# Kernel tuning notes

Measured on AMD Instinct MI355X. Metric: run time of the kernel, lower is better.

The kernel has to match this reference:

```python
import jax, jax.numpy as jnp
import numpy as np

H = 1024      # hidden_dim == memory_dim (required by seq-axis concat)
M = 1024      # memory_dim
FF = 4096     # ff_dim
WIN = 16      # window_size
SLOTS = 10    # persistent memory slots
B, S = 2, 4096
EPS_LN = 1e-5
EPS_NORM = 1e-12


def _layernorm(x, g, b):
    m = jnp.mean(x, axis=-1, keepdims=True)
    v = jnp.var(x, axis=-1, keepdims=True)
    return (x - m) / jnp.sqrt(v + EPS_LN) * g + b


def setup_inputs() -> dict:
    key = jax.random.key(0)
    ks = jax.random.split(key, 12)

    def lin_w(k, out_d, in_d):
        return jax.random.normal(k, (out_d, in_d), jnp.float32) / np.sqrt(in_d)

    return {
        "x": jax.random.normal(ks[0], (B, S, H), jnp.float32),
        "mem_W": lin_w(ks[1], M, M), "mem_b": jnp.zeros((M,), jnp.float32),
        "P": jax.random.normal(ks[2], (SLOTS, M), jnp.float32),
        "Wi": lin_w(ks[3], M, H), "bi": jnp.zeros((M,), jnp.float32),
        "Wl1": lin_w(ks[4], M, M), "bl1": jnp.zeros((M,), jnp.float32),
        "Wl2": lin_w(ks[5], M, M), "bl2": jnp.zeros((M,), jnp.float32),
        "Wo": lin_w(ks[6], H, M), "bo": jnp.zeros((H,), jnp.float32),
        "fgate": jnp.ones((1,), jnp.float32),
        "lrate": jnp.ones((1,), jnp.float32),
        "Wg": lin_w(ks[7], H, 2 * H), "bg": jnp.zeros((H,), jnp.float32),
        "W1": lin_w(ks[8], FF, H), "b1": jnp.zeros((FF,), jnp.float32),
        "W2": lin_w(ks[9], H, FF), "b2": jnp.zeros((H,), jnp.float32),
        "g1": jnp.ones((H,), jnp.float32), "be1": jnp.zeros((H,), jnp.float32),
        "g2": jnp.ones((H,), jnp.float32), "be2": jnp.zeros((H,), jnp.float32),
        "g3": jnp.ones((H,), jnp.float32), "be3": jnp.zeros((H,), jnp.float32),
    }


def reference(x, mem_W, mem_b, P, Wi, bi, Wl1, bl1, Wl2, bl2, Wo, bo,
              fgate, lrate, Wg, bg, W1, b1, W2, b2,
              g1, be1, g2, be2, g3, be3):
    b, s, h = x.shape
    # k = concat(x, persistent) along seq; v = k.clone()
    k_full = jnp.concatenate([x, jnp.broadcast_to(P, (b,) + P.shape)], axis=1)  # [B, S+SLOTS, H]

    # sit at positions >= S and are never inside the window, so only x is attended.
    idx = jnp.arange(s)[:, None] + jnp.arange(-WIN, 1)[None, :]
    valid = idx >= 0
    k_win = k_full[:, jnp.maximum(idx, 0)]
    scores = jnp.einsum('bsh,bswh->bsw', x, k_win) * (h ** -0.5)
    scores = jnp.where(valid[None], scores, -jnp.inf)
    attn_out = jnp.einsum('bsw,bswh->bsh', jax.nn.softmax(scores, axis=-1), k_win)
    x1 = _layernorm(x + attn_out, g1, be1)

    # --- neural long-term memory (key == value since v = k.clone())
    kv = k_full.reshape(-1, h)
    kn = kv / jnp.maximum(jnp.linalg.norm(kv, axis=-1, keepdims=True), EPS_NORM)
    kp = kn @ Wi.T + bi          # projected key; value_proj is identical
    vp = kp
    hdd = jax.nn.silu(kp @ Wl1.T + bl1)
    hdd = jax.nn.silu(hdd @ Wl2.T + bl2)
    pred = hdd @ mem_W.T + mem_b
    diff = pred - vp
    n, m = diff.shape
    grad_W = (2.0 / (n * m)) * diff.T @ hdd          # d mse / d mem_W
    W_new = (1.0 - fgate) * mem_W + lrate * grad_W   # test-time memory update
    mem_out = hdd @ W_new.T + mem_b
    mo = (mem_out @ Wo.T + bo).reshape(b, -1, h)[:, :s]  # align with x seq length

    # --- gated fusion + FFN
    gate = jax.nn.sigmoid(jnp.concatenate([x1, mo], axis=-1) @ Wg.T + bg)
    combined = gate * x1 + (1.0 - gate) * mo
    x2 = _layernorm(x1 + combined, g2, be2)
    ff = jax.nn.silu(x2 @ W1.T + b1) @ W2.T + b2
    return _layernorm(x2 + ff, g3, be3)
```

## Files before the change

kernel.cpp:

```cpp
#include <hip/hip_runtime.h>
#include <hip/hip_bf16.h>

#define WIN 16
#define SLOTS 10
#define SS 4096
#define NTOK 8192
#define NKV 8212
#define NPOS 4106

typedef unsigned short u16;
typedef unsigned int u32;
typedef __attribute__((ext_vector_type(8))) short short8;
typedef __attribute__((ext_vector_type(4))) float f32x4;

__device__ __forceinline__ u16 f2bf(float f){
  union { float f; u32 u; } a; a.f = f;
  u32 r = (a.u + 0x7fff + ((a.u >> 16) & 1)) >> 16;
  return (u16)r;
}
__device__ __forceinline__ float bf2f(u16 v){
  union { u32 u; float f; } a; a.u = ((u32)v) << 16;
  return a.f;
}

#define GLOAD(gp, lp) __builtin_amdgcn_global_load_lds( \
    (const __attribute__((address_space(1))) void*)(gp), \
    (__attribute__((address_space(3))) void*)(lp), 16, 0, 0)

#define FENCE_BARRIER() do { \
    __builtin_amdgcn_sched_barrier(0); \
    __builtin_amdgcn_s_barrier(); \
    __builtin_amdgcn_sched_barrier(0); \
  } while(0)

__global__ __launch_bounds__(256) void cvt_all(
    const float4* __restrict__ s0, const float4* __restrict__ s1,
    const float4* __restrict__ s2, const float4* __restrict__ s3,
    const float4* __restrict__ s4, const float4* __restrict__ s5,
    const float4* __restrict__ s6, const float4* __restrict__ s7,
    ushort4* __restrict__ d0, ushort4* __restrict__ d1,
    ushort4* __restrict__ d2, ushort4* __restrict__ d3,
    ushort4* __restrict__ d4, ushort4* __restrict__ d5,
    ushort4* __restrict__ d6, ushort4* __restrict__ d7)
{
  int i = blockIdx.x * 256 + threadIdx.x;
  const float4* s; ushort4* d; int base;
  if      (i <  262144){ s=s0; d=d0; base=0; }
  else if (i <  524288){ s=s1; d=d1; base=262144; }
  else if (i <  786432){ s=s2; d=d2; base=524288; }
  else if (i < 1048576){ s=s3; d=d3; base=786432; }
  else if (i < 1310720){ s=s4; d=d4; base=1048576; }
  else if (i < 1835008){ s=s5; d=d5; base=1310720; }
  else if (i < 2883584){ s=s6; d=d6; base=1835008; }
  else                 { s=s7; d=d7; base=2883584; }
  float4 v = s[i - base];
  ushort4 o; o.x=f2bf(v.x); o.y=f2bf(v.y); o.z=f2bf(v.z); o.w=f2bf(v.w);
  d[i - base] = o;
}

__global__ __launch_bounds__(256) void attn_ln1(
    const float* __restrict__ x, const float* __restrict__ g1,
    const float* __restrict__ be1, u16* __restrict__ x1b)
{
  const int n = blockIdx.x;
  const int b = n >> 12, s = n & 4095;
  const int t = threadIdx.x, lane = t & 63, w = t >> 6;
  const float* xb = x + ((size_t)b << 22);
  const float4 q = ((const float4*)(xb + ((size_t)s << 10)))[t];
  const int j0 = (s >= WIN) ? 0 : (WIN - s);
  float kvv[17][4];
  float part[17];
  #pragma unroll
  for (int j=0;j<17;j++){
    float4 kk = make_float4(0.f,0.f,0.f,0.f);
    if (j >= j0) kk = ((const float4*)(xb + ((size_t)(s - WIN + j) << 10)))[t];
    kvv[j][0]=kk.x; kvv[j][1]=kk.y; kvv[j][2]=kk.z; kvv[j][3]=kk.w;
    part[j] = q.x*kk.x + q.y*kk.y + q.z*kk.z + q.w*kk.w;
  }
  __shared__ float red[17][4];
  #pragma unroll
  for (int j=0;j<17;j++){
    float v = part[j];
    #pragma unroll
    for (int off=32; off; off>>=1) v += __shfl_xor(v, off, 64);
    if (lane == 0) red[j][w] = v;
  }
  __syncthreads();
  __shared__ float wsh[17];
  if (t == 0){
    float sc[17];
    float mx = -3.0e38f;
    #pragma unroll
    for (int j=0;j<17;j++){
      float v = (red[j][0]+red[j][1]+red[j][2]+red[j][3]) * 0.03125f;
      sc[j] = v;
      if (j >= j0) mx = fmaxf(mx, v);
    }
    float ssum = 0.f;
    #pragma unroll
    for (int j=0;j<17;j++){
      float e = (j >= j0) ? expf(sc[j]-mx) : 0.f;
      wsh[j] = e; ssum += e;
    }
    float inv = 1.f/ssum;
    #pragma unroll
    for (int j=0;j<17;j++) wsh[j] *= inv;
  }
  __syncthreads();
  float y0=q.x, y1=q.y, y2=q.z, y3=q.w;
  #pragma unroll
  for (int j=0;j<17;j++){
    float wj = wsh[j];
    y0 += wj*kvv[j][0]; y1 += wj*kvv[j][1]; y2 += wj*kvv[j][2]; y3 += wj*kvv[j][3];
  }
  float s1 = y0+y1+y2+y3;
  float s2 = y0*y0+y1*y1+y2*y2+y3*y3;
  #pragma unroll
  for (int off=32; off; off>>=1){ s1 += __shfl_xor(s1, off, 64); s2 += __shfl_xor(s2, off, 64); }
  __shared__ float rsh[8];
  if (lane == 0){ rsh[w] = s1; rsh[4+w] = s2; }
  __syncthreads();
  float S1 = rsh[0]+rsh[1]+rsh[2]+rsh[3];
  float S2 = rsh[4]+rsh[5]+rsh[6]+rsh[7];
  float mean = S1 * (1.f/1024.f);
  float var  = S2 * (1.f/1024.f) - mean*mean;
  float rstd = 1.f/sqrtf(var + 1e-5f);
  float4 gv = ((const float4*)g1)[t];
  float4 bv = ((const float4*)be1)[t];
  ushort4 ob;
  ob.x = f2bf((y0-mean)*rstd*gv.x + bv.x);
  ob.y = f2bf((y1-mean)*rstd*gv.y + bv.y);
  ob.z = f2bf((y2-mean)*rstd*gv.z + bv.z);
  ob.w = f2bf((y3-mean)*rstd*gv.w + bv.w);
  ((ushort4*)x1b)[((size_t)n << 8) + t] = ob;
}

__global__ __launch_bounds__(256) void kv_norm(const float* __restrict__ x,
                                               const float* __restrict__ P,
                                               u16* __restrict__ kn)
{
  const int r = blockIdx.x;
  const int t = threadIdx.x, lane = t & 63, w = t >> 6;
  const int b = r / NPOS;
  const int pos = r - b*NPOS;
  const float* src = (pos < SS) ? (x + (((size_t)b*SS + pos) << 10))
                                : (P + ((size_t)(pos - SS) << 10));
  float4 v = ((const float4*)src)[t];
  float s2 = v.x*v.x + v.y*v.y + v.z*v.z + v.w*v.w;
  #pragma unroll
  for (int off=32; off; off>>=1) s2 += __shfl_xor(s2, off, 64);
  __shared__ float sh[4];
  if (lane == 0) sh[w] = s2;
  __syncthreads();
  float S = sh[0]+sh[1]+sh[2]+sh[3];
  float inv = 1.f / fmaxf(sqrtf(S), 1e-12f);
  ushort4 o; o.x=f2bf(v.x*inv); o.y=f2bf(v.y*inv); o.z=f2bf(v.z*inv); o.w=f2bf(v.w*inv);
  ((ushort4*)kn)[((size_t)r << 8) + t] = o;
}

template<int EPI, int SPLITA>
__global__ __launch_bounds__(256) void gemm_nt(
    const u16* __restrict__ A, const u16* __restrict__ A2,
    const u16* __restrict__ Bmat, const float* __restrict__ bias,
    const u16* __restrict__ auxb,
    float* __restrict__ Cf, u16* __restrict__ Cb,
    int N, int O, int ldA, int ldB, int klen)
{
  __shared__ __align__(16) u16 lA[2][128*64];
  __shared__ __align__(16) u16 lB[2][128*64];
  const int t = threadIdx.x;
  const int lane = t & 63;
  const int bm0 = blockIdx.x * 128;
  const int bn0 = blockIdx.y * 128;
  const int wid = t >> 6;
  const int wr = wid >> 1, wc = wid & 1;
  const int nkt = klen >> 6;

  f32x4 acc[4][4];
  #pragma unroll
  for (int i=0;i<4;i++)
    #pragma unroll
    for (int j=0;j<4;j++)
      acc[i][j] = (f32x4){0.f,0.f,0.f,0.f};

  const int srow = t >> 3;
  const int schunk = (((t & 7) ^ (srow & 7)) << 3);

  const u16* baseA[4]; const u16* baseA2[4]; const u16* baseB[4];
  #pragma unroll
  for (int i=0;i<4;i++){
    int gr = bm0 + srow + i*32; gr = gr < N ? gr : N-1;
    baseA[i] = A + (size_t)gr*(size_t)ldA + schunk;
    if (SPLITA) baseA2[i] = A2 + ((size_t)gr << 10) + schunk;
    int gb = bn0 + srow + i*32; gb = gb < O ? gb : O-1;
    baseB[i] = Bmat + (size_t)gb*(size_t)ldB + schunk;
  }

  auto stage = [&](int kt, int buf){
    const int kb = kt << 6;
    #pragma unroll
    for (int i=0;i<4;i++){
      const u16* src = SPLITA ? ((kb < 1024) ? baseA[i] + kb : baseA2[i] + (kb - 1024))
                              : baseA[i] + kb;
      GLOAD(src, &lA[buf][(i*256 + t) << 3]);
    }
    #pragma unroll
    for (int i=0;i<4;i++)
      GLOAD(baseB[i] + kb, &lB[buf][(i*256 + t) << 3]);
  };

  stage(0, 0);
  if (nkt > 1) stage(1, 1);

  const int l15 = lane & 15;
  const int rx = l15 & 7;
  const int cq = lane >> 4;

  for (int kt = 0; kt < nkt; ++kt){
    const int cur = kt & 1;
    if (kt + 1 < nkt) { asm volatile("s_waitcnt vmcnt(8)" ::: "memory"); }
    else              { asm volatile("s_waitcnt vmcnt(0)" ::: "memory"); }
    FENCE_BARRIER();
    #pragma unroll
    for (int kk=0;kk<2;kk++){
      const int soff = (((kk*4 + cq) ^ rx) << 3);
      short8 af[4], bfv[4];
      #pragma unroll
      for (int mi=0;mi<4;mi++)
        af[mi] = *(const short8*)(&lA[cur][((wr*64 + mi*16 + l15) << 6) + soff]);
      #pragma unroll
      for (int ni=0;ni<4;ni++)
        bfv[ni] = *(const short8*)(&lB[cur][((wc*64 + ni*16 + l15) << 6) + soff]);
      #pragma unroll
      for (int mi=0;mi<4;mi++)
        #pragma unroll
        for (int ni=0;ni<4;ni++)
          acc[mi][ni] = __builtin_amdgcn_mfma_f32_16x16x32_bf16(af[mi], bfv[ni], acc[mi][ni], 0, 0, 0);
    }
    FENCE_BARRIER();
    if (kt + 2 < nkt) stage(kt + 2, cur);
  }

  const int rbase = (lane >> 4) * 4;
  const int cidx = lane & 15;
  #pragma unroll
  for (int mi=0;mi<4;mi++){
    #pragma unroll
    for (int r=0;r<4;r++){
      const int n = bm0 + wr*64 + mi*16 + rbase + r;
      if (n >= N) continue;
      #pragma unroll
      for (int ni=0;ni<4;ni++){
        const int o = bn0 + wc*64 + ni*16 + cidx;
        float v = acc[mi][ni][r] + bias[o];
        if (EPI == 6){
          int b = n / NPOS;
          int pos = n - b*NPOS;
          if (pos < SS){
            Cb[(((size_t)(b*SS + pos)) << 10) + o] = f2bf(v);
          }
        } else {
          size_t idx = (size_t)n*(size_t)O + o;
          if (EPI == 0){ Cf[idx] = v; }
          else if (EPI == 1){ float sv = v/(1.f+__expf(-v)); Cb[idx] = f2bf(sv); }
          else if (EPI == 2){ Cb[idx] = f2bf(v); }
          else if (EPI == 4){ Cb[idx] = f2bf(v - bf2f(auxb[idx])); }
          else if (EPI == 5){ Cb[idx] = f2bf(1.f/(1.f+__expf(-v))); }
        }
      }
    }
  }
}

template<int EPI>
__global__ __launch_bounds__(512, 2) void gemm_256(
    const u16* __restrict__ A, const u16* __restrict__ Bmat,
    const float* __restrict__ bias,
    float* __restrict__ Cf, u16* __restrict__ Cb,
    int N, int O, int ldA, int ldB, int klen)
{
  __shared__ __align__(16) u16 lA[4][256*32];
  __shared__ __align__(16) u16 lB[4][256*32];
  const int t = threadIdx.x;
  const int lane = t & 63;
  const int wid = t >> 6;
  const int wr = wid >> 2, wc = wid & 3;
  const int bm0 = blockIdx.x * 256;
  const int bn0 = blockIdx.y * 256;
  const int nkh = (klen >> 6) * 2;

  f32x4 acc[8][4];
  #pragma unroll
  for (int i=0;i<8;i++)
    #pragma unroll
    for (int j=0;j<4;j++)
      acc[i][j] = (f32x4){0.f,0.f,0.f,0.f};

  const int srow = t >> 2;
  const int sch  = t & 3;
  const int csw  = ((sch ^ ((srow >> 1) & 3)) << 3);
  int gr0 = bm0 + srow;       gr0 = gr0 < N ? gr0 : N-1;
  int gr1 = bm0 + srow + 128; gr1 = gr1 < N ? gr1 : N-1;
  int gb0 = bn0 + srow;       gb0 = gb0 < O ? gb0 : O-1;
  int gb1 = bn0 + srow + 128; gb1 = gb1 < O ? gb1 : O-1;
  const u16* baseA0 = A    + (size_t)gr0*(size_t)ldA + csw;
  const u16* baseA1 = A    + (size_t)gr1*(size_t)ldA + csw;
  const u16* baseB0 = Bmat + (size_t)gb0*(size_t)ldB + csw;
  const u16* baseB1 = Bmat + (size_t)gb1*(size_t)ldB + csw;
  const int ldsLo = srow*32 + (sch << 3);
  const int ldsHi = (srow + 128)*32 + (sch << 3);

  auto stageA = [&](int j){
    const int kb = j << 5;
    const int s = j & 3;
    GLOAD(baseA0 + kb, &lA[s][ldsLo]);
    GLOAD(baseA1 + kb, &lA[s][ldsHi]);
  };
  auto stageB = [&](int j){
    const int kb = j << 5;
    const int s = j & 3;
    GLOAD(baseB0 + kb, &lB[s][ldsLo]);
    GLOAD(baseB1 + kb, &lB[s][ldsHi]);
  };

  stageA(0); stageB(0);
  if (nkh > 1){ stageA(1); stageB(1); }
  if (nkh > 2){ stageA(2); stageB(2); }

  const int l15 = lane & 15;
  const int cq  = lane >> 4;
  const int chS = ((cq ^ ((l15 >> 1) & 3)) << 3);

  for (int j = 0; j < nkh; ++j){
    const int s = j & 3;
    const int rem = nkh - 1 - j;
    if (rem >= 2)      { asm volatile("s_waitcnt vmcnt(8)" ::: "memory"); }
    else if (rem == 1) { asm volatile("s_waitcnt vmcnt(4)" ::: "memory"); }
    else               { asm volatile("s_waitcnt vmcnt(0)" ::: "memory"); }
    FENCE_BARRIER();
    short8 af[4], bfv[4];
    #pragma unroll
    for (int ni=0;ni<4;ni++)
      bfv[ni] = *(const short8*)(&lB[s][((wc*64 + ni*16 + l15) * 32) + chS]);
    #pragma unroll
    for (int mi=0;mi<4;mi++)
      af[mi] = *(const short8*)(&lA[s][((wr*128 + mi*16 + l15) * 32) + chS]);
    if (j + 3 < nkh) stageA(j + 3);
    __builtin_amdgcn_sched_barrier(0);
    __builtin_amdgcn_s_setprio(1);
    #pragma unroll
    for (int mi=0;mi<4;mi++)
      #pragma unroll
      for (int ni=0;ni<4;ni++)
        acc[mi][ni] = __builtin_amdgcn_mfma_f32_16x16x32_bf16(af[mi], bfv[ni], acc[mi][ni], 0, 0, 0);
    __builtin_amdgcn_s_setprio(0);
    __builtin_amdgcn_sched_barrier(0);
    FENCE_BARRIER();
    #pragma unroll
    for (int mi=0;mi<4;mi++)
      af[mi] = *(const short8*)(&lA[s][((wr*128 + (mi+4)*16 + l15) * 32) + chS]);
    if (j + 3 < nkh) stageB(j + 3);
    __builtin_amdgcn_sched_barrier(0);
    __builtin_amdgcn_s_setprio(1);
    #pragma unroll
    for (int mi=0;mi<4;mi++)
      #pragma unroll
      for (int ni=0;ni<4;ni++)
        acc[mi+4][ni] = __builtin_amdgcn_mfma_f32_16x16x32_bf16(af[mi], bfv[ni], acc[mi+4][ni], 0, 0, 0);
    __builtin_amdgcn_s_setprio(0);
    __builtin_amdgcn_sched_barrier(0);
  }

  const int rbase = (lane >> 4) * 4;
  const int cidx = lane & 15;
  #pragma unroll
  for (int mi=0;mi<8;mi++){
    #pragma unroll
    for (int r=0;r<4;r++){
      const int n = bm0 + wr*128 + mi*16 + rbase + r;
      if (n >= N) continue;
      #pragma unroll
      for (int ni=0;ni<4;ni++){
        const int o = bn0 + wc*64 + ni*16 + cidx;
        float v = acc[mi][ni][r] + bias[o];
        size_t idx = (size_t)n*(size_t)O + o;
        if (EPI == 0){ Cf[idx] = v; }
        else if (EPI == 1){ float sv = v/(1.f+__expf(-v)); Cb[idx] = f2bf(sv); }
        else if (EPI == 2){ Cb[idx] = f2bf(v); }
      }
    }
  }
}

#define NSPLIT 6
__global__ __launch_bounds__(256) void gemm_tn(
    const u16* __restrict__ A, const u16* __restrict__ B,
    float* __restrict__ part0, float* __restrict__ part1)
{
  __shared__ __align__(16) u16 lA[128*64];
  __shared__ __align__(16) u16 lB[128*64];
  const int t = threadIdx.x, lane = t & 63;
  const int i0 = blockIdx.x * 128, j0 = blockIdx.y * 128, z = blockIdx.z;
  const int wid = t >> 6, wr = wid >> 1, wc = wid & 1;
  const int TILES = (NKV + 63) >> 6;
  const int PER = (TILES + NSPLIT - 1) / NSPLIT;
  const int kt0 = z * PER;
  const int ktend = (kt0 + PER < TILES) ? (kt0 + PER) : TILES;

  f32x4 acc[4][4];
  #pragma unroll
  for (int i=0;i<4;i++)
    #pragma unroll
    for (int j=0;j<4;j++)
      acc[i][j] = (f32x4){0.f,0.f,0.f,0.f};

  const int p = t & 31;
  const int g = t >> 5;

  auto loadr = [&](int kt, short8 R[8]){
    const int n0 = kt << 6;
    const int na = n0 + 2*p, nb = na + 1;
    short8 z8 = (short8){0,0,0,0,0,0,0,0};
    R[0]=z8;R[1]=z8;R[2]=z8;R[3]=z8;R[4]=z8;R[5]=z8;R[6]=z8;R[7]=z8;
    if (na < NKV){
      const u16* ra = A + (size_t)na*1024 + i0 + g*16;
      R[0] = *(const short8*)ra; R[1] = *(const short8*)(ra+8);
      const u16* rb = B + (size_t)na*1024 + j0 + g*16;
      R[4] = *(const short8*)rb; R[5] = *(const short8*)(rb+8);
    }
    if (nb < NKV){
      const u16* ra = A + (size_t)nb*1024 + i0 + g*16;
      R[2] = *(const short8*)ra; R[3] = *(const short8*)(ra+8);
      const u16* rb = B + (size_t)nb*1024 + j0 + g*16;
      R[6] = *(const short8*)rb; R[7] = *(const short8*)(rb+8);
    }
  };

  short8 cr[8], nr[8];
  loadr(kt0, cr);

  const int pc = p >> 2, pl = p & 3;

  for (int kt = kt0; kt < ktend; ++kt){
    if (kt + 1 < ktend) loadr(kt + 1, nr);
    asm volatile("" ::: "memory");
    FENCE_BARRIER();
    u32* wA = (u32*)lA; u32* wB = (u32*)lB;
    #pragma unroll
    for (int e=0;e<8;e++){
      const int s = (pc ^ e) * 4 + pl;
      wA[(g*16 + e)*32 + s]     = ((u32)(u16)cr[0][e]) | (((u32)(u16)cr[2][e]) << 16);
      wB[(g*16 + e)*32 + s]     = ((u32)(u16)cr[4][e]) | (((u32)(u16)cr[6][e]) << 16);
    }
    #pragma unroll
    for (int e=0;e<8;e++){
      const int s = (pc ^ e) * 4 + pl;
      wA[(g*16 + 8 + e)*32 + s] = ((u32)(u16)cr[1][e]) | (((u32)(u16)cr[3][e]) << 16);
      wB[(g*16 + 8 + e)*32 + s] = ((u32)(u16)cr[5][e]) | (((u32)(u16)cr[7][e]) << 16);
    }
    asm volatile("s_waitcnt lgkmcnt(0)" ::: "memory");
    FENCE_BARRIER();
    const int l15 = lane & 15;
    const int rx = l15 & 7;
    const int cq = lane >> 4;
    #pragma unroll
    for (int kk=0;kk<2;kk++){
      const int soff = (((kk*4 + cq) ^ rx) << 3);
      short8 af[4], bfv[4];
      #pragma unroll
      for (int mi=0;mi<4;mi++)
        af[mi] = *(const short8*)(lA + ((wr*64 + mi*16 + l15) << 6) + soff);
      #pragma unroll
      for (int ni=0;ni<4;ni++)
        bfv[ni] = *(const short8*)(lB + ((wc*64 + ni*16 + l15) << 6) + soff);
      #pragma unroll
      for (int mi=0;mi<4;mi++)
        #pragma unroll
        for (int ni=0;ni<4;ni++)
          acc[mi][ni] = __builtin_amdgcn_mfma_f32_16x16x32_bf16(af[mi], bfv[ni], acc[mi][ni], 0, 0, 0);
    }
    #pragma unroll
    for (int e=0;e<8;e++) cr[e] = nr[e];
  }

  float* dst = (z < 4) ? (part0 + ((size_t)z << 20)) : (part1 + ((size_t)(z-4) << 20));
  const int rbase = (lane >> 4) * 4;
  const int cidx = lane & 15;
  #pragma unroll
  for (int mi=0;mi<4;mi++)
    #pragma unroll
    for (int r=0;r<4;r++){
      const int i = i0 + wr*64 + mi*16 + rbase + r;
      #pragma unroll
      for (int ni=0;ni<4;ni++){
        const int j = j0 + wc*64 + ni*16 + cidx;
        dst[((size_t)i << 10) + j] = acc[mi][ni][r];
      }
    }
}

__global__ __launch_bounds__(256) void wnew_k(const float* __restrict__ part0,
                                              const float* __restrict__ part1,
                                              const float* __restrict__ memW,
                                              const float* __restrict__ fg,
                                              const float* __restrict__ lr,
                                              u16* __restrict__ out)
{
  int i = blockIdx.x*256 + threadIdx.x;
  float s = part0[i] + part0[i + (1<<20)] + part0[i + (2<<20)] + part0[i + (3<<20)]
          + part1[i] + part1[i + (1<<20)];
  const float scale = 2.f / ((float)NKV * 1024.f);
  float v = (1.f - fg[0])*memW[i] + lr[0]*scale*s;
  out[i] = f2bf(v);
}

__global__ __launch_bounds__(256) void ln_gate(
    const u16* __restrict__ x1b, const u16* __restrict__ gateb,
    const u16* __restrict__ mob, const float* __restrict__ g2,
    const float* __restrict__ be2, u16* __restrict__ x2b)
{
  const int n = blockIdx.x;
  const int t = threadIdx.x, lane = t & 63, w = t >> 6;
  const size_t rb = (size_t)n << 8;
  ushort4 xa = ((const ushort4*)x1b)[rb+t];
  ushort4 ga = ((const ushort4*)gateb)[rb+t];
  ushort4 ma = ((const ushort4*)mob)[rb+t];
  float a0=bf2f(xa.x),a1=bf2f(xa.y),a2=bf2f(xa.z),a3=bf2f(xa.w);
  float g0=bf2f(ga.x),g1v=bf2f(ga.y),g2v=bf2f(ga.z),g3v=bf2f(ga.w);
  float m0=bf2f(ma.x),m1=bf2f(ma.y),m2=bf2f(ma.z),m3=bf2f(ma.w);
  float y0 = a0 + g0*a0 + (1.f-g0)*m0;
  float y1 = a1 + g1v*a1 + (1.f-g1v)*m1;
  float y2 = a2 + g2v*a2 + (1.f-g2v)*m2;
  float y3 = a3 + g3v*a3 + (1.f-g3v)*m3;
  float s1 = y0+y1+y2+y3;
  float s2 = y0*y0+y1*y1+y2*y2+y3*y3;
  #pragma unroll
  for (int off=32; off; off>>=1){ s1 += __shfl_xor(s1, off, 64); s2 += __shfl_xor(s2, off, 64); }
  __shared__ float rsh[8];
  if (lane == 0){ rsh[w] = s1; rsh[4+w] = s2; }
  __syncthreads();
  float S1 = rsh[0]+rsh[1]+rsh[2]+rsh[3];
  float S2 = rsh[4]+rsh[5]+rsh[6]+rsh[7];
  float mean = S1 * (1.f/1024.f);
  float var  = S2 * (1.f/1024.f) - mean*mean;
  float rstd = 1.f/sqrtf(var + 1e-5f);
  float4 gv = ((const float4*)g2)[t];
  float4 bv = ((const float4*)be2)[t];
  ushort4 ob;
  ob.x = f2bf((y0-mean)*rstd*gv.x + bv.x);
  ob.y = f2bf((y1-mean)*rstd*gv.y + bv.y);
  ob.z = f2bf((y2-mean)*rstd*gv.z + bv.z);
  ob.w = f2bf((y3-mean)*rstd*gv.w + bv.w);
  ((ushort4*)x2b)[rb + t] = ob;
}

__global__ __launch_bounds__(256) void ln_final(
    const u16* __restrict__ x2b, const float* __restrict__ g3,
    const float* __restrict__ be3, float* __restrict__ out)
{
  const int n = blockIdx.x;
  const int t = threadIdx.x, lane = t & 63, w = t >> 6;
  const size_t rb = (size_t)n << 8;
  ushort4 xa = ((const ushort4*)x2b)[rb+t];
  float4 f = ((const float4*)out)[rb+t];
  float y0 = bf2f(xa.x)+f.x, y1 = bf2f(xa.y)+f.y, y2 = bf2f(xa.z)+f.z, y3 = bf2f(xa.w)+f.w;
  float s1 = y0+y1+y2+y3;
  float s2 = y0*y0+y1*y1+y2*y2+y3*y3;
  #pragma unroll
  for (int off=32; off; off>>=1){ s1 += __shfl_xor(s1, off, 64); s2 += __shfl_xor(s2, off, 64); }
  __shared__ float rsh[8];
  if (lane == 0){ rsh[w] = s1; rsh[4+w] = s2; }
  __syncthreads();
  float S1 = rsh[0]+rsh[1]+rsh[2]+rsh[3];
  float S2 = rsh[4]+rsh[5]+rsh[6]+rsh[7];
  float mean = S1 * (1.f/1024.f);
  float var  = S2 * (1.f/1024.f) - mean*mean;
  float rstd = 1.f/sqrtf(var + 1e-5f);
  float4 gv = ((const float4*)g3)[t];
  float4 bv = ((const float4*)be3)[t];
  float4 o;
  o.x = (y0-mean)*rstd*gv.x + bv.x;
  o.y = (y1-mean)*rstd*gv.y + bv.y;
  o.z = (y2-mean)*rstd*gv.z + bv.z;
  o.w = (y3-mean)*rstd*gv.w + bv.w;
  ((float4*)out)[rb + t] = o;
}

extern "C" void kernel_launch(void* const* d_in, const int* in_sizes, int n_in,
                              void* d_out, int out_size, void* d_ws, size_t ws_size,
                              hipStream_t stream)
{
  const float* x    = (const float*)d_in[0];
  const float* memW = (const float*)d_in[1];
  const float* memb = (const float*)d_in[2];
  const float* P    = (const float*)d_in[3];
  const float* Wi   = (const float*)d_in[4];
  const float* bi   = (const float*)d_in[5];
  const float* Wl1  = (const float*)d_in[6];
  const float* bl1  = (const float*)d_in[7];
  const float* Wl2  = (const float*)d_in[8];
  const float* bl2  = (const float*)d_in[9];
  const float* Wo   = (const float*)d_in[10];
  const float* bo   = (const float*)d_in[11];
  const float* fg   = (const float*)d_in[12];
  const float* lr   = (const float*)d_in[13];
  const float* Wg   = (const float*)d_in[14];
  const float* bg   = (const float*)d_in[15];
  const float* W1   = (const float*)d_in[16];
  const float* b1   = (const float*)d_in[17];
  const float* W2   = (const float*)d_in[18];
  const float* b2   = (const float*)d_in[19];
  const float* g1   = (const float*)d_in[20];
  const float* be1  = (const float*)d_in[21];
  const float* g2   = (const float*)d_in[22];
  const float* be2  = (const float*)d_in[23];
  const float* g3   = (const float*)d_in[24];
  const float* be3  = (const float*)d_in[25];
  float* out = (float*)d_out;

  const size_t SZ_TOK = (size_t)NTOK*1024*2;
  const size_t SZ_KV  = (size_t)NKV*1024*2;
  char* base = (char*)d_ws;
  size_t off = 0;
  auto alloc = [&](size_t bytes) -> char* {
    char* p = base + off;
    off += (bytes + 255) & ~(size_t)255;
    return p;
  };
  u16* x1b   = (u16*)alloc(SZ_TOK);
  u16* knb   = (u16*)alloc(SZ_KV);
  u16* h1b   = (u16*)alloc(SZ_KV);
  u16* hddb  = (u16*)alloc(SZ_KV);
  u16* kpb   = (u16*)alloc(SZ_KV);
  u16* wnewb = (u16*)alloc((size_t)1024*1024*2);
  u16* WiB   = (u16*)alloc((size_t)1024*1024*2);
  u16* Wl1B  = (u16*)alloc((size_t)1024*1024*2);
  u16* Wl2B  = (u16*)alloc((size_t)1024*1024*2);
  u16* memWB = (u16*)alloc((size_t)1024*1024*2);
  u16* WoB   = (u16*)alloc((size_t)1024*1024*2);
  u16* WgB   = (u16*)alloc((size_t)1024*2048*2);
  u16* W1B   = (u16*)alloc((size_t)4096*1024*2);
  u16* W2B   = (u16*)alloc((size_t)1024*4096*2);
  if (ws_size < off) return;

  u16*   diffb   = knb;
  float* part0   = (float*)kpb;
  float* part1   = (float*)WiB;
  u16*   memoutb = knb;
  u16*   mob     = h1b;
  u16*   gateb   = hddb;
  u16*   x2b     = kpb;
  u16*   ff1b    = x1b;

  cvt_all<<<15360, 256, 0, stream>>>(
      (const float4*)Wi, (const float4*)Wl1, (const float4*)Wl2, (const float4*)memW,
      (const float4*)Wo, (const float4*)Wg, (const float4*)W1, (const float4*)W2,
      (ushort4*)WiB, (ushort4*)Wl1B, (ushort4*)Wl2B, (ushort4*)memWB,
      (ushort4*)WoB, (ushort4*)WgB, (ushort4*)W1B, (ushort4*)W2B);

  attn_ln1<<<NTOK, 256, 0, stream>>>(x, g1, be1, x1b);
  kv_norm <<<NKV,  256, 0, stream>>>(x, P, knb);

  dim3 gkv(65, 8, 1);
  gemm_nt<2,0><<<gkv, 256, 0, stream>>>(knb, nullptr, WiB, bi, nullptr, nullptr, kpb, NKV, 1024, 1024, 1024, 1024);
  gemm_nt<1,0><<<gkv, 256, 0, stream>>>(kpb, nullptr, Wl1B, bl1, nullptr, nullptr, h1b, NKV, 1024, 1024, 1024, 1024);
  gemm_nt<1,0><<<gkv, 256, 0, stream>>>(h1b, nullptr, Wl2B, bl2, nullptr, nullptr, hddb, NKV, 1024, 1024, 1024, 1024);
  gemm_nt<4,0><<<gkv, 256, 0, stream>>>(hddb, nullptr, memWB, memb, kpb, nullptr, diffb, NKV, 1024, 1024, 1024, 1024);
  gemm_tn<<<dim3(8, 8, NSPLIT), 256, 0, stream>>>(diffb, hddb, part0, part1);
  wnew_k<<<4096, 256, 0, stream>>>(part0, part1, memW, fg, lr, wnewb);
  gemm_nt<2,0><<<gkv, 256, 0, stream>>>(hddb, nullptr, wnewb, memb, nullptr, nullptr, memoutb, NKV, 1024, 1024, 1024, 1024);
  gemm_nt<6,0><<<gkv, 256, 0, stream>>>(memoutb, nullptr, WoB, bo, nullptr, nullptr, mob, NKV, 1024, 1024, 1024, 1024);
  gemm_nt<5,1><<<dim3(64, 8, 1), 256, 0, stream>>>(x1b, mob, WgB, bg, nullptr, nullptr, gateb, NTOK, 1024, 1024, 2048, 2048);
  ln_gate<<<NTOK, 256, 0, stream>>>(x1b, gateb, mob, g2, be2, x2b);
  gemm_256<1><<<dim3(32, 16, 1), 512, 0, stream>>>(x2b, W1B, b1, nullptr, ff1b, NTOK, 4096, 1024, 1024, 1024);
  gemm_nt<0,0><<<dim3(64, 8, 1), 256, 0, stream>>>(ff1b, nullptr, W2B, b2, nullptr, out, nullptr, NTOK, 1024, 4096, 4096, 4096);
  ln_final<<<NTOK, 256, 0, stream>>>(x2b, g3, be3, out);
}
```

Before: 633.7 us.

## Deepen gemm_nt pipeline to 4 stages and merge attention with kv norm

The main bf16 GEMM moves from a double-buffered loop with 64-wide K tiles to a 4-stage ring of 32-wide K tiles. Each iteration now has a single barrier, the next prefetch is issued right after the LDS fragment reads, and the MFMA block runs at raised wave priority. The goal is to hide global-load latency and cut synchronisation stalls, at the cost of twice as many loop iterations per K and a new swizzle. Separately, the attention+LN1 and key-normalisation kernels are merged into one launch that branches on block index, removing a launch and letting the two run concurrently.

Measured after the change: 630.3 us. About the same (-0.5%).

```diff
diff --git a/kernel.cpp b/kernel.cpp
--- a/kernel.cpp
+++ b/kernel.cpp
@@ -58,13 +58,34 @@
   d[i - base] = o;
 }
 
-__global__ __launch_bounds__(256) void attn_ln1(
-    const float* __restrict__ x, const float* __restrict__ g1,
-    const float* __restrict__ be1, u16* __restrict__ x1b)
-{
-  const int n = blockIdx.x;
+__global__ __launch_bounds__(256) void attn_kv(
+    const float* __restrict__ x, const float* __restrict__ P,
+    const float* __restrict__ g1, const float* __restrict__ be1,
+    u16* __restrict__ x1b, u16* __restrict__ kn)
+{
+  const int blk = blockIdx.x;
+  const int t = threadIdx.x, lane = t & 63, w = t >> 6;
+  if (blk >= NTOK){
+    const int r = blk - NTOK;
+    const int b = r / NPOS;
+    const int pos = r - b*NPOS;
+    const float* src = (pos < SS) ? (x + (((size_t)b*SS + pos) << 10))
+                                  : (P + ((size_t)(pos - SS) << 10));
+    float4 v = ((const float4*)src)[t];
+    float s2 = v.x*v.x + v.y*v.y + v.z*v.z + v.w*v.w;
+    #pragma unroll
+    for (int off=32; off; off>>=1) s2 += __shfl_xor(s2, off, 64);
+    __shared__ float sh[4];
+    if (lane == 0) sh[w] = s2;
+    __syncthreads();
+    float S = sh[0]+sh[1]+sh[2]+sh[3];
+    float inv = 1.f / fmaxf(sqrtf(S), 1e-12f);
+    ushort4 o; o.x=f2bf(v.x*inv); o.y=f2bf(v.y*inv); o.z=f2bf(v.z*inv); o.w=f2bf(v.w*inv);
+    ((ushort4*)kn)[((size_t)r << 8) + t] = o;
+    return;
+  }
+  const int n = blk;
   const int b = n >> 12, s = n & 4095;
-  const int t = threadIdx.x, lane = t & 63, w = t >> 6;
   const float* xb = x + ((size_t)b << 22);
   const float4 q = ((const float4*)(xb + ((size_t)s << 10)))[t];
   const int j0 = (s >= WIN) ? 0 : (WIN - s);
@@ -135,29 +156,6 @@
   ((ushort4*)x1b)[((size_t)n << 8) + t] = ob;
 }
 
-__global__ __launch_bounds__(256) void kv_norm(const float* __restrict__ x,
-                                               const float* __restrict__ P,
-                                               u16* __restrict__ kn)
-{
-  const int r = blockIdx.x;
-  const int t = threadIdx.x, lane = t & 63, w = t >> 6;
-  const int b = r / NPOS;
-  const int pos = r - b*NPOS;
-  const float* src = (pos < SS) ? (x + (((size_t)b*SS + pos) << 10))
-                                : (P + ((size_t)(pos - SS) << 10));
-  float4 v = ((const float4*)src)[t];
-  float s2 = v.x*v.x + v.y*v.y + v.z*v.z + v.w*v.w;
-  #pragma unroll
-  for (int off=32; off; off>>=1) s2 += __shfl_xor(s2, off, 64);
-  __shared__ float sh[4];
-  if (lane == 0) sh[w] = s2;
-  __syncthreads();
-  float S = sh[0]+sh[1]+sh[2]+sh[3];
-  float inv = 1.f / fmaxf(sqrtf(S), 1e-12f);
-  ushort4 o; o.x=f2bf(v.x*inv); o.y=f2bf(v.y*inv); o.z=f2bf(v.z*inv); o.w=f2bf(v.w*inv);
-  ((ushort4*)kn)[((size_t)r << 8) + t] = o;
-}
-
 template<int EPI, int SPLITA>
 __global__ __launch_bounds__(256) void gemm_nt(
     const u16* __restrict__ A, const u16* __restrict__ A2,
@@ -166,15 +164,15 @@
     float* __restrict__ Cf, u16* __restrict__ Cb,
     int N, int O, int ldA, int ldB, int klen)
 {
-  __shared__ __align__(16) u16 lA[2][128*64];
-  __shared__ __align__(16) u16 lB[2][128*64];
+  __shared__ __align__(16) u16 lA[4][128*32];
+  __shared__ __align__(16) u16 lB[4][128*32];
   const int t = threadIdx.x;
   const int lane = t & 63;
   const int bm0 = blockIdx.x * 128;
   const int bn0 = blockIdx.y * 128;
   const int wid = t >> 6;
   const int wr = wid >> 1, wc = wid & 1;
-  const int nkt = klen >> 6;
+  const int nkh = klen >> 5;
 
   f32x4 acc[4][4];
   #pragma unroll
@@ -183,62 +181,66 @@
     for (int j=0;j<4;j++)
       acc[i][j] = (f32x4){0.f,0.f,0.f,0.f};
 
-  const int srow = t >> 3;
-  const int schunk = (((t & 7) ^ (srow & 7)) << 3);
-
-  const u16* baseA[4]; const u16* baseA2[4]; const u16* baseB[4];
-  #pragma unroll
-  for (int i=0;i<4;i++){
-    int gr = bm0 + srow + i*32; gr = gr < N ? gr : N-1;
-    baseA[i] = A + (size_t)gr*(size_t)ldA + schunk;
-    if (SPLITA) baseA2[i] = A2 + ((size_t)gr << 10) + schunk;
-    int gb = bn0 + srow + i*32; gb = gb < O ? gb : O-1;
-    baseB[i] = Bmat + (size_t)gb*(size_t)ldB + schunk;
-  }
-
-  auto stage = [&](int kt, int buf){
-    const int kb = kt << 6;
-    #pragma unroll
-    for (int i=0;i<4;i++){
-      const u16* src = SPLITA ? ((kb < 1024) ? baseA[i] + kb : baseA2[i] + (kb - 1024))
-                              : baseA[i] + kb;
-      GLOAD(src, &lA[buf][(i*256 + t) << 3]);
-    }
-    #pragma unroll
-    for (int i=0;i<4;i++)
-      GLOAD(baseB[i] + kb, &lB[buf][(i*256 + t) << 3]);
+  const int srow = t >> 2;
+  const int sch  = t & 3;
+  const int csw  = ((sch ^ ((srow >> 1) & 3)) << 3);
+
+  int gr0 = bm0 + srow;      gr0 = gr0 < N ? gr0 : N-1;
+  int gr1 = bm0 + srow + 64; gr1 = gr1 < N ? gr1 : N-1;
+  int gb0 = bn0 + srow;      gb0 = gb0 < O ? gb0 : O-1;
+  int gb1 = bn0 + srow + 64; gb1 = gb1 < O ? gb1 : O-1;
+  const u16* bA0 = A + (size_t)gr0*(size_t)ldA + csw;
+  const u16* bA1 = A + (size_t)gr1*(size_t)ldA + csw;
+  const u16* bA20 = SPLITA ? (A2 + ((size_t)gr0 << 10) + csw) : nullptr;
+  const u16* bA21 = SPLITA ? (A2 + ((size_t)gr1 << 10) + csw) : nullptr;
+  const u16* bB0 = Bmat + (size_t)gb0*(size_t)ldB + csw;
+  const u16* bB1 = Bmat + (size_t)gb1*(size_t)ldB + csw;
+  const int dLo = t << 3;
+  const int dHi = (t << 3) + 2048;
+
+  auto stage = [&](int j){
+    const int kb = j << 5;
+    const int s = j & 3;
+    const u16* a0 = SPLITA ? ((kb < 1024) ? bA0 + kb : bA20 + (kb - 1024)) : bA0 + kb;
+    const u16* a1 = SPLITA ? ((kb < 1024) ? bA1 + kb : bA21 + (kb - 1024)) : bA1 + kb;
+    GLOAD(a0, &lA[s][dLo]);
+    GLOAD(a1, &lA[s][dHi]);
+    GLOAD(bB0 + kb, &lB[s][dLo]);
+    GLOAD(bB1 + kb, &lB[s][dHi]);
   };
 
-  stage(0, 0);
-  if (nkt > 1) stage(1, 1);
+  stage(0);
+  if (nkh > 1) stage(1);
+  if (nkh > 2) stage(2);
 
   const int l15 = lane & 15;
-  const int rx = l15 & 7;
-  const int cq = lane >> 4;
-
-  for (int kt = 0; kt < nkt; ++kt){
-    const int cur = kt & 1;
-    if (kt + 1 < nkt) { asm volatile("s_waitcnt vmcnt(8)" ::: "memory"); }
-    else              { asm volatile("s_waitcnt vmcnt(0)" ::: "memory"); }
+  const int cq  = lane >> 4;
+  const int soff = ((cq ^ ((l15 >> 1) & 3)) << 3);
+
+  for (int j = 0; j < nkh; ++j){
+    const int s = j & 3;
+    const int cnt = 4*((j+1 < nkh) + (j+2 < nkh));
+    if (cnt == 8)      { asm volatile("s_waitcnt vmcnt(8)" ::: "memory"); }
+    else if (cnt == 4) { asm volatile("s_waitcnt vmcnt(4)" ::: "memory"); }
+    else               { asm volatile("s_waitcnt vmcnt(0)" ::: "memory"); }
     FENCE_BARRIER();
-    #pragma unroll
-    for (int kk=0;kk<2;kk++){
-      const int soff = (((kk*4 + cq) ^ rx) << 3);
-      short8 af[4], bfv[4];
-      #pragma unroll
-      for (int mi=0;mi<4;mi++)
-        af[mi] = *(const short8*)(&lA[cur][((wr*64 + mi*16 + l15) << 6) + soff]);
+    short8 af[4], bfv[4];
+    #pragma unroll
+    for (int mi=0;mi<4;mi++)
+      af[mi] = *(const short8*)(&lA[s][((wr*64 + mi*16 + l15) * 32) + soff]);
+    #pragma unroll
+    for (int ni=0;ni<4;ni++)
+      bfv[ni] = *(const short8*)(&lB[s][((wc*64 + ni*16 + l15) * 32) + soff]);
+    if (j + 3 < nkh) stage(j + 3);
+    __builtin_amdgcn_sched_barrier(0);
+    __builtin_amdgcn_s_setprio(1);
+    #pragma unroll
+    for (int mi=0;mi<4;mi++)
       #pragma unroll
       for (int ni=0;ni<4;ni++)
-        bfv[ni] = *(const short8*)(&lB[cur][((wc*64 + ni*16 + l15) << 6) + soff]);
-      #pragma unroll
-      for (int mi=0;mi<4;mi++)
-        #pragma unroll
-        for (int ni=0;ni<4;ni++)
-          acc[mi][ni] = __builtin_amdgcn_mfma_f32_16x16x32_bf16(af[mi], bfv[ni], acc[mi][ni], 0, 0, 0);
-    }
-    FENCE_BARRIER();
-    if (kt + 2 < nkt) stage(kt + 2, cur);
+        acc[mi][ni] = __builtin_amdgcn_mfma_f32_16x16x32_bf16(af[mi], bfv[ni], acc[mi][ni], 0, 0, 0);
+    __builtin_amdgcn_s_setprio(0);
+    __builtin_amdgcn_sched_barrier(0);
   }
 
   const int rbase = (lane >> 4) * 4;
@@ -658,8 +660,7 @@
       (ushort4*)WiB, (ushort4*)Wl1B, (ushort4*)Wl2B, (ushort4*)memWB,
       (ushort4*)WoB, (ushort4*)WgB, (ushort4*)W1B, (ushort4*)W2B);
 
-  attn_ln1<<<NTOK, 256, 0, stream>>>(x, g1, be1, x1b);
-  kv_norm <<<NKV,  256, 0, stream>>>(x, P, knb);
+  attn_kv<<<NTOK + NKV, 256, 0, stream>>>(x, P, g1, be1, x1b, knb);
 
   dim3 gkv(65, 8, 1);
   gemm_nt<2,0><<<gkv, 256, 0, stream>>>(knb, nullptr, WiB, bi, nullptr, nullptr, kpb, NKV, 1024, 1024, 1024, 1024);
```
